# Performance work log

Hardware: AMD Instinct MI355X
Metric: run time of the kernel (lower is better)

## Reference

```python
import jax, jax.numpy as jnp
import numpy as np

B, T, L, D, H = 8, 4, 512, 512, 8
HD = D // H
THR = 1.0
BETA = 0.5
EPS = 1e-5


def heaviside(x):
    return (x >= 0).astype(x.dtype)


def bn_eval(x, g, b, rm, rv):
    # BatchNorm1d in eval mode applied on the last dim
    return (x - rm) * (g * jax.lax.rsqrt(rv + EPS)) + b


def lif(x_btld):
    # snntorch Leaky(beta=0.5, threshold=1, reset='subtract'), mem init 0, scan over T
    xs = jnp.moveaxis(x_btld, 1, 0)  # (T,B,L,D)

    def step(mem, xt):
        reset = heaviside(mem - THR)          # reset from previous mem (detached in torch)
        mem = BETA * mem + xt - reset * THR
        spk = heaviside(mem - THR)
        return mem, spk

    _, spks = jax.lax.scan(step, jnp.zeros_like(xs[0]), xs)
    return jnp.moveaxis(spks, 0, 1)


def setup_inputs() -> dict:
    key = jax.random.key(0)
    ks = jax.random.split(key, 24)
    s = D ** -0.5
    inp = {
        "x": jax.random.normal(ks[0], (B, T, L, D), jnp.float32),
        "q_w": jax.random.normal(ks[1], (D, D), jnp.float32) * s,
        "q_g": jax.random.normal(ks[2], (D,), jnp.float32),
        "q_b": jax.random.normal(ks[3], (D,), jnp.float32),
        "q_rm": jax.random.normal(ks[4], (D,), jnp.float32),
        "q_rv": jax.random.uniform(ks[5], (D,), jnp.float32),
        "k_w": jax.random.normal(ks[6], (D, D), jnp.float32) * s,
        "k_g": jax.random.normal(ks[7], (D,), jnp.float32),
        "k_b": jax.random.normal(ks[8], (D,), jnp.float32),
        "k_rm": jax.random.normal(ks[9], (D,), jnp.float32),
        "k_rv": jax.random.uniform(ks[10], (D,), jnp.float32),
        "v_w": jax.random.normal(ks[11], (D, D), jnp.float32) * s,
        "v_g": jax.random.normal(ks[12], (D,), jnp.float32),
        "v_b": jax.random.normal(ks[13], (D,), jnp.float32),
        "v_rm": jax.random.normal(ks[14], (D,), jnp.float32),
        "v_rv": jax.random.uniform(ks[15], (D,), jnp.float32),
        "o_w": jax.random.normal(ks[16], (D, D), jnp.float32) * s,
        "o_bias": jax.random.normal(ks[17], (D,), jnp.float32),
        "o_g": jax.random.normal(ks[18], (D,), jnp.float32),
        "o_b": jax.random.normal(ks[19], (D,), jnp.float32),
        "o_rm": jax.random.normal(ks[20], (D,), jnp.float32),
        "o_rv": jax.random.uniform(ks[21], (D,), jnp.float32),
    }
    return inp


def reference(x, q_w, q_g, q_b, q_rm, q_rv, k_w, k_g, k_b, k_rm, k_rv,
              v_w, v_g, v_b, v_rm, v_rv, o_w, o_bias, o_g, o_b, o_rm, o_rv):
    scale = HD ** -0.5
    # Q path: linear -> BN -> LIF (binary {0,1})
    q = bn_eval(jnp.einsum('btld,ed->btle', x, q_w), q_g, q_b, q_rm, q_rv)
    q = lif(q)
    # K path: linear -> BN -> ReLU (continuous)
    k = jax.nn.relu(bn_eval(jnp.einsum('btld,ed->btle', x, k_w), k_g, k_b, k_rm, k_rv))
    # V path: linear -> BN -> ternary {-1,0,+1}
    v = bn_eval(jnp.einsum('btld,ed->btle', x, v_w), v_g, v_b, v_rm, v_rv)
    v = heaviside(v - THR) - heaviside(-v - THR)
    # split heads: (B,T,H,L,hd)
    sh = lambda a: a.reshape(B, T, L, H, HD).transpose(0, 1, 3, 2, 4)
    q, k, v = sh(q), sh(k), sh(v)
    attn = jnp.einsum('bthld,bthmd->bthlm', q, k) * scale
    out = jnp.einsum('bthlm,bthmd->bthld', attn, v)
    out = out.transpose(0, 1, 3, 2, 4).reshape(B, T, L, D)
    out = jnp.einsum('btld,ed->btle', out, o_w) + o_bias
    out = bn_eval(out, o_g, o_b, o_rm, o_rv)
    return lif(out)
```

## Files before the change

kernel.cpp:

```cpp
#include <hip/hip_runtime.h>
#include <math.h>
#include <stdint.h>

#define Bb 8
#define Tt 4
#define Ll 512
#define Dd 512
#define Hh 8
#define HDd 64
#define Mm (Bb*Tt*Ll)

typedef _Float16 f16;
typedef _Float16 f16x8 __attribute__((ext_vector_type(8)));
typedef float f32x4 __attribute__((ext_vector_type(4)));

#define LO_SCALE 2048.0f
#define LO_INV   4.8828125e-4f

__device__ __forceinline__ void gload16(const void* g, void* l) {
  __builtin_amdgcn_global_load_lds(
      (const __attribute__((address_space(1))) unsigned int*)(uintptr_t)g,
      (__attribute__((address_space(3))) unsigned int*)(uintptr_t)l,
      16, 0, 0);
}

struct SplitArgs {
  const float* src[5];
  f16* hi[5];
  f16* lo[5];
};

__global__ void split_k(SplitArgs s) {
  int i = blockIdx.x * 256 + threadIdx.x;
  int seg, base;
  if (i < 1048576) { seg = 0; base = i; }
  else { int r = i - 1048576; seg = 1 + (r >> 15); base = r & 32767; }
  const float* sp = s.src[seg] + (size_t)base * 8;
  float4 v0 = *(const float4*)sp;
  float4 v1 = *(const float4*)(sp + 4);
  float a[8] = {v0.x, v0.y, v0.z, v0.w, v1.x, v1.y, v1.z, v1.w};
  f16x8 hv, lv;
  #pragma unroll
  for (int e = 0; e < 8; ++e) {
    f16 hh = (f16)a[e];
    hv[e] = hh;
    lv[e] = (f16)((a[e] - (float)hh) * LO_SCALE);
  }
  *(f16x8*)(s.hi[seg] + (size_t)base * 8) = hv;
  *(f16x8*)(s.lo[seg] + (size_t)base * 8) = lv;
}

struct GArgs {
  const f16 *Ah, *Al;
  const f16 *Wh0, *Wl0, *Wh1, *Wl1, *Wh2, *Wl2;
  const float *g0,*b0,*rm0,*rv0;
  const float *g1,*b1,*rm1,*rv1;
  const float *g2,*b2,*rm2,*rv2;
  const float* bias;
  float *o0, *o1, *o2;
};

template<int MODE>
__global__ __launch_bounds__(256, 2)
void gemm_f16(GArgs ar) {
  __shared__ __align__(16) f16 Ah_s[4096];
  __shared__ __align__(16) f16 Al_s[4096];
  __shared__ __align__(16) f16 Bh_s[4096];
  __shared__ __align__(16) f16 Bl_s[4096];

  const int tid = threadIdx.x;
  const int lane = tid & 63, wid = tid >> 6;
  const int bx = blockIdx.x, by = blockIdx.y;
  const int seg = (MODE == 0) ? (bx >> 2) : 0;
  const int lc0 = (MODE == 0) ? ((bx & 3) << 7) : (bx << 7);
  const int m0 = by << 7;

  const f16* Wh = (seg == 0 ? ar.Wh0 : (seg == 1 ? ar.Wh1 : ar.Wh2));
  const f16* Wl = (seg == 0 ? ar.Wl0 : (seg == 1 ? ar.Wl1 : ar.Wl2));
  const float* gp  = (seg == 0 ? ar.g0  : (seg == 1 ? ar.g1  : ar.g2));
  const float* bp  = (seg == 0 ? ar.b0  : (seg == 1 ? ar.b1  : ar.b2));
  const float* rmp = (seg == 0 ? ar.rm0 : (seg == 1 ? ar.rm1 : ar.rm2));
  const float* rvp = (seg == 0 ? ar.rv0 : (seg == 1 ? ar.rv1 : ar.rv2));
  float* outp = (seg == 0 ? ar.o0 : (seg == 1 ? ar.o1 : ar.o2));

  const int srow = lane >> 2, skc = lane & 3;
  const int fr = lane & 15, kg = lane >> 4;
  const int wmr = wid >> 1, wnc = wid & 1;

  f32x4 acc_h[4][4], acc_l[4][4];
  #pragma unroll
  for (int i = 0; i < 4; ++i)
    #pragma unroll
    for (int j = 0; j < 4; ++j) {
      acc_h[i][j] = (f32x4)0.0f;
      acc_l[i][j] = (f32x4)0.0f;
    }

  for (int k0 = 0; k0 < Dd; k0 += 32) {
    __syncthreads();
    #pragma unroll
    for (int i = 0; i < 2; ++i) {
      const int r = i * 64 + wid * 16 + srow;
      const size_t goA = (size_t)(m0 + r) * Dd + k0 + skc * 8;
      const size_t goB = (size_t)(lc0 + r) * Dd + k0 + skc * 8;
      const int lbase = i * 2048 + wid * 512;
      gload16(ar.Ah + goA, Ah_s + lbase);
      gload16(ar.Al + goA, Al_s + lbase);
      gload16(Wh + goB, Bh_s + lbase);
      gload16(Wl + goB, Bl_s + lbase);
    }
    __syncthreads();

    f16x8 a_h[4], a_l[4], b_h[4], b_l[4];
    #pragma unroll
    for (int i = 0; i < 4; ++i) {
      const int ra = (wmr * 64 + i * 16 + fr) * 32 + kg * 8;
      a_h[i] = *(const f16x8*)&Ah_s[ra];
      a_l[i] = *(const f16x8*)&Al_s[ra];
      const int rb = (wnc * 64 + i * 16 + fr) * 32 + kg * 8;
      b_h[i] = *(const f16x8*)&Bh_s[rb];
      b_l[i] = *(const f16x8*)&Bl_s[rb];
    }
    #pragma unroll
    for (int i = 0; i < 4; ++i)
      #pragma unroll
      for (int j = 0; j < 4; ++j) {
        acc_h[i][j] = __builtin_amdgcn_mfma_f32_16x16x32_f16(a_h[i], b_h[j], acc_h[i][j], 0, 0, 0);
        acc_l[i][j] = __builtin_amdgcn_mfma_f32_16x16x32_f16(a_h[i], b_l[j], acc_l[i][j], 0, 0, 0);
        acc_l[i][j] = __builtin_amdgcn_mfma_f32_16x16x32_f16(a_l[i], b_h[j], acc_l[i][j], 0, 0, 0);
      }
  }

  float scl[4], shc[4];
  #pragma unroll
  for (int j = 0; j < 4; ++j) {
    const int c = lc0 + wnc * 64 + j * 16 + fr;
    double S = (double)gp[c] / sqrt((double)rvp[c] + 1e-5);
    double Sh = (double)bp[c] - (double)rmp[c] * S;
    if (MODE == 1) Sh += (double)ar.bias[c] * S;
    scl[j] = (float)S; shc[j] = (float)Sh;
  }

  #pragma unroll
  for (int i = 0; i < 4; ++i)
    #pragma unroll
    for (int r = 0; r < 4; ++r) {
      const int row = m0 + wmr * 64 + i * 16 + kg * 4 + r;
      #pragma unroll
      for (int j = 0; j < 4; ++j) {
        const int col = lc0 + wnc * 64 + j * 16 + fr;
        float val = acc_h[i][j][r] + acc_l[i][j][r] * LO_INV;
        float y = val * scl[j] + shc[j];
        if (MODE == 0) {
          if (seg == 1) y = fmaxf(y, 0.f);
          else if (seg == 2) y = (y >= 1.f ? 1.f : 0.f) - (-y >= 1.f ? 1.f : 0.f);
        }
        outp[(size_t)row * Dd + col] = y;
      }
    }
}

__global__ void lif_k(float* __restrict__ buf) {
  const int N4 = Bb * Ll * Dd / 4;
  int i = blockIdx.x * blockDim.x + threadIdx.x;
  if (i >= N4) return;
  const int PB = Ll * Dd / 4;
  int b = i >> 16;
  int r = i & 65535;
  float4* p0 = (float4*)buf + (size_t)b * Tt * PB + r;
  float m0 = 0.f, m1 = 0.f, m2 = 0.f, m3 = 0.f;
  #pragma unroll
  for (int t = 0; t < Tt; ++t) {
    float4* p = p0 + (size_t)t * PB;
    float4 xv = *p;
    float4 s;
    { float rst = (m0 >= 1.f) ? 1.f : 0.f; m0 = 0.5f * m0 + xv.x - rst; s.x = (m0 >= 1.f) ? 1.f : 0.f; }
    { float rst = (m1 >= 1.f) ? 1.f : 0.f; m1 = 0.5f * m1 + xv.y - rst; s.y = (m1 >= 1.f) ? 1.f : 0.f; }
    { float rst = (m2 >= 1.f) ? 1.f : 0.f; m2 = 0.5f * m2 + xv.z - rst; s.z = (m2 >= 1.f) ? 1.f : 0.f; }
    { float rst = (m3 >= 1.f) ? 1.f : 0.f; m3 = 0.5f * m3 + xv.w - rst; s.w = (m3 >= 1.f) ? 1.f : 0.f; }
    *p = s;
  }
}

__global__ __launch_bounds__(256)
void attn_g(const float* __restrict__ ks, const float* __restrict__ vs,
            float* __restrict__ pG) {
  const int bt = blockIdx.x, h = blockIdx.y, c = blockIdx.z;
  const float* kp = ks + (size_t)bt * Ll * Dd + h * HDd;
  const float* vp = vs + (size_t)bt * Ll * Dd + h * HDd;

  __shared__ float KS[64][68];
  __shared__ float VS[64][68];
  const int tid = threadIdx.x;
  const int te = tid & 15, td = tid >> 4;

  float gacc[4][4];
  #pragma unroll
  for (int i = 0; i < 4; ++i)
    #pragma unroll
    for (int j = 0; j < 4; ++j) gacc[i][j] = 0.f;

  for (int mt = 0; mt < 2; ++mt) {
    const int m0 = c * 128 + mt * 64;
    #pragma unroll
    for (int it = 0; it < 4; ++it) {
      int fidx = it * 256 + tid;
      int row = fidx >> 4, fq = fidx & 15;
      *(float4*)&KS[row][fq << 2] = *(const float4*)(kp + (size_t)(m0 + row) * Dd + (fq << 2));
      *(float4*)&VS[row][fq << 2] = *(const float4*)(vp + (size_t)(m0 + row) * Dd + (fq << 2));
    }
    __syncthreads();
    #pragma unroll 4
    for (int mm = 0; mm < 64; ++mm) {
      float4 k4 = *(const float4*)&KS[mm][te << 2];
      float4 v4 = *(const float4*)&VS[mm][td << 2];
      const float kk[4] = {k4.x, k4.y, k4.z, k4.w};
      const float vv[4] = {v4.x, v4.y, v4.z, v4.w};
      #pragma unroll
      for (int i = 0; i < 4; ++i)
        #pragma unroll
        for (int j = 0; j < 4; ++j)
          gacc[i][j] = fmaf(kk[i], vv[j], gacc[i][j]);
    }
    __syncthreads();
  }
  float* out = pG + (((size_t)(bt * 8 + h) * 4 + c) << 12);
  #pragma unroll
  for (int i = 0; i < 4; ++i)
    *(float4*)&out[((te << 2) + i) * 64 + (td << 2)] =
        make_float4(gacc[i][0] * 0.125f, gacc[i][1] * 0.125f,
                    gacc[i][2] * 0.125f, gacc[i][3] * 0.125f);
}

__global__ __launch_bounds__(256)
void attn_o(const float* __restrict__ qs, const float* __restrict__ pG,
            f16* __restrict__ ahi, f16* __restrict__ alo) {
  const int bt = blockIdx.x, h = blockIdx.y, lc = blockIdx.z;
  __shared__ float G[64][68];
  __shared__ float QS[64][68];
  const int tid = threadIdx.x;

  const float* pg = pG + (((size_t)(bt * 8 + h) * 4) << 12);
  #pragma unroll
  for (int rep = 0; rep < 4; ++rep) {
    int t4 = rep * 256 + tid;
    int e = t4 >> 4, dq = t4 & 15;
    int off = e * 64 + (dq << 2);
    float4 s0 = *(const float4*)(pg + off);
    float4 s1 = *(const float4*)(pg + 4096 + off);
    float4 s2 = *(const float4*)(pg + 8192 + off);
    float4 s3 = *(const float4*)(pg + 12288 + off);
    *(float4*)&G[e][dq << 2] = make_float4(s0.x + s1.x + s2.x + s3.x,
                                           s0.y + s1.y + s2.y + s3.y,
                                           s0.z + s1.z + s2.z + s3.z,
                                           s0.w + s1.w + s2.w + s3.w);
  }
  __syncthreads();

  const float* qp = qs + (size_t)bt * Ll * Dd + h * HDd;
  const int lr = tid >> 2, dg = tid & 3;

  for (int l0 = 0; l0 < 128; l0 += 64) {
    #pragma unroll
    for (int it = 0; it < 4; ++it) {
      int fidx = it * 256 + tid;
      int row = fidx >> 4, fq = fidx & 15;
      *(float4*)&QS[row][fq << 2] =
          *(const float4*)(qp + (size_t)(lc * 128 + l0 + row) * Dd + (fq << 2));
    }
    __syncthreads();
    float oacc[16];
    #pragma unroll
    for (int j = 0; j < 16; ++j) oacc[j] = 0.f;
    for (int ee = 0; ee < 64; ++ee) {
      float qv = QS[lr][ee];
      #pragma unroll
      for (int jq = 0; jq < 4; ++jq) {
        float4 g4 = *(const float4*)&G[ee][(dg << 4) + (jq << 2)];
        oacc[jq * 4 + 0] = fmaf(qv, g4.x, oacc[jq * 4 + 0]);
        oacc[jq * 4 + 1] = fmaf(qv, g4.y, oacc[jq * 4 + 1]);
        oacc[jq * 4 + 2] = fmaf(qv, g4.z, oacc[jq * 4 + 2]);
        oacc[jq * 4 + 3] = fmaf(qv, g4.w, oacc[jq * 4 + 3]);
      }
    }
    f16x8 h0, l0v, h1, l1v;
    #pragma unroll
    for (int t = 0; t < 8; ++t) {
      float v = oacc[t];
      f16 hh = (f16)v;
      h0[t] = hh; l0v[t] = (f16)((v - (float)hh) * LO_SCALE);
      float v2 = oacc[8 + t];
      f16 hh2 = (f16)v2;
      h1[t] = hh2; l1v[t] = (f16)((v2 - (float)hh2) * LO_SCALE);
    }
    size_t ob = ((size_t)bt * Ll + lc * 128 + l0 + lr) * Dd + h * HDd + (dg << 4);
    *(f16x8*)(ahi + ob) = h0;
    *(f16x8*)(ahi + ob + 8) = h1;
    *(f16x8*)(alo + ob) = l0v;
    *(f16x8*)(alo + ob + 8) = l1v;
    __syncthreads();
  }
}

extern "C" void kernel_launch(void* const* d_in, const int* in_sizes, int n_in,
                              void* d_out, int out_size, void* d_ws, size_t ws_size,
                              hipStream_t stream) {
  const float* x    = (const float*)d_in[0];
  const float* q_w  = (const float*)d_in[1];
  const float* q_g  = (const float*)d_in[2];
  const float* q_b  = (const float*)d_in[3];
  const float* q_rm = (const float*)d_in[4];
  const float* q_rv = (const float*)d_in[5];
  const float* k_w  = (const float*)d_in[6];
  const float* k_g  = (const float*)d_in[7];
  const float* k_b  = (const float*)d_in[8];
  const float* k_rm = (const float*)d_in[9];
  const float* k_rv = (const float*)d_in[10];
  const float* v_w  = (const float*)d_in[11];
  const float* v_g  = (const float*)d_in[12];
  const float* v_b  = (const float*)d_in[13];
  const float* v_rm = (const float*)d_in[14];
  const float* v_rv = (const float*)d_in[15];
  const float* o_w  = (const float*)d_in[16];
  const float* o_bias = (const float*)d_in[17];
  const float* o_g  = (const float*)d_in[18];
  const float* o_b  = (const float*)d_in[19];
  const float* o_rm = (const float*)d_in[20];
  const float* o_rv = (const float*)d_in[21];

  float* ws = (float*)d_ws;
  const size_t NBUF = (size_t)Mm * Dd;
  float* q_lin = ws;
  float* kbuf  = ws + NBUF;
  float* vbuf  = ws + 2 * NBUF;
  float* reg3  = ws + 3 * NBUF;
  f16* xhi = (f16*)reg3;
  f16* xlo = xhi + NBUF;
  float* pG = reg3;
  f16* wsp = (f16*)(ws + 4 * NBUF);
  f16* qwh = wsp;            f16* qwl = wsp + 262144;
  f16* kwh = wsp + 2*262144; f16* kwl = wsp + 3*262144;
  f16* vwh = wsp + 4*262144; f16* vwl = wsp + 5*262144;
  f16* owh = wsp + 6*262144; f16* owl = wsp + 7*262144;
  f16* ahi = (f16*)kbuf;
  f16* alo = ahi + NBUF;
  float* obuf = (float*)d_out;

  SplitArgs sa;
  sa.src[0] = x;   sa.hi[0] = xhi; sa.lo[0] = xlo;
  sa.src[1] = q_w; sa.hi[1] = qwh; sa.lo[1] = qwl;
  sa.src[2] = k_w; sa.hi[2] = kwh; sa.lo[2] = kwl;
  sa.src[3] = v_w; sa.hi[3] = vwh; sa.lo[3] = vwl;
  sa.src[4] = o_w; sa.hi[4] = owh; sa.lo[4] = owl;
  split_k<<<4608, 256, 0, stream>>>(sa);

  GArgs a1;
  a1.Ah = xhi; a1.Al = xlo;
  a1.Wh0 = qwh; a1.Wl0 = qwl; a1.Wh1 = kwh; a1.Wl1 = kwl; a1.Wh2 = vwh; a1.Wl2 = vwl;
  a1.g0 = q_g; a1.b0 = q_b; a1.rm0 = q_rm; a1.rv0 = q_rv;
  a1.g1 = k_g; a1.b1 = k_b; a1.rm1 = k_rm; a1.rv1 = k_rv;
  a1.g2 = v_g; a1.b2 = v_b; a1.rm2 = v_rm; a1.rv2 = v_rv;
  a1.bias = nullptr;
  a1.o0 = q_lin; a1.o1 = kbuf; a1.o2 = vbuf;
  gemm_f16<0><<<dim3(12, 128), 256, 0, stream>>>(a1);

  lif_k<<<2048, 256, 0, stream>>>(q_lin);

  attn_g<<<dim3(32, 8, 4), 256, 0, stream>>>(kbuf, vbuf, pG);
  attn_o<<<dim3(32, 8, 4), 256, 0, stream>>>(q_lin, pG, ahi, alo);

  GArgs a2;
  a2.Ah = ahi; a2.Al = alo;
  a2.Wh0 = owh; a2.Wl0 = owl; a2.Wh1 = owh; a2.Wl1 = owl; a2.Wh2 = owh; a2.Wl2 = owl;
  a2.g0 = o_g; a2.b0 = o_b; a2.rm0 = o_rm; a2.rv0 = o_rv;
  a2.g1 = o_g; a2.b1 = o_b; a2.rm1 = o_rm; a2.rv1 = o_rv;
  a2.g2 = o_g; a2.b2 = o_b; a2.rm2 = o_rm; a2.rv2 = o_rv;
  a2.bias = o_bias;
  a2.o0 = obuf; a2.o1 = obuf; a2.o2 = obuf;
  gemm_f16<1><<<dim3(4, 128), 256, 0, stream>>>(a2);

  lif_k<<<2048, 256, 0, stream>>>(obuf);
}
```

Before: 313.0 us.

## Fuse LIF scan into GEMM epilogues and store binary spikes as fp16

Each GEMM block's M tile is remapped so it covers all 4 timesteps of 32 L-rows for one batch. The LIF recurrence can then run in the epilogue through a shared-memory transpose, and the two standalone lif_k passes are removed. Q spikes and ternary V are stored as fp16 instead of fp32, which cuts write and read traffic for the attention kernels. This costs extra shared memory, added barriers and an LDS transpose in the epilogue, and A-row loads are no longer contiguous 128-row blocks.

```diff
diff --git a/kernel.cpp b/kernel.cpp
--- a/kernel.cpp
+++ b/kernel.cpp
@@ -12,6 +12,7 @@
 
 typedef _Float16 f16;
 typedef _Float16 f16x8 __attribute__((ext_vector_type(8)));
+typedef _Float16 f16x4 __attribute__((ext_vector_type(4)));
 typedef float f32x4 __attribute__((ext_vector_type(4)));
 
 #define LO_SCALE 2048.0f
@@ -57,23 +58,30 @@
   const float *g1,*b1,*rm1,*rv1;
   const float *g2,*b2,*rm2,*rv2;
   const float* bias;
-  float *o0, *o1, *o2;
+  f16*   oq;
+  float* ok;
+  f16*   ov;
+  float* oo;
 };
+
+#define SMEM_BYTES 34048
 
 template<int MODE>
 __global__ __launch_bounds__(256, 2)
 void gemm_f16(GArgs ar) {
-  __shared__ __align__(16) f16 Ah_s[4096];
-  __shared__ __align__(16) f16 Al_s[4096];
-  __shared__ __align__(16) f16 Bh_s[4096];
-  __shared__ __align__(16) f16 Bl_s[4096];
+  extern __shared__ __align__(16) char smem[];
+  f16* Ah_s = (f16*)smem;
+  f16* Al_s = (f16*)(smem + 8192);
+  f16* Bh_s = (f16*)(smem + 16384);
+  f16* Bl_s = (f16*)(smem + 24576);
+  float (*TS)[133] = (float(*)[133])smem;
 
   const int tid = threadIdx.x;
   const int lane = tid & 63, wid = tid >> 6;
   const int bx = blockIdx.x, by = blockIdx.y;
   const int seg = (MODE == 0) ? (bx >> 2) : 0;
   const int lc0 = (MODE == 0) ? ((bx & 3) << 7) : (bx << 7);
-  const int m0 = by << 7;
+  const int b = by >> 4, lc32 = by & 15;
 
   const f16* Wh = (seg == 0 ? ar.Wh0 : (seg == 1 ? ar.Wh1 : ar.Wh2));
   const f16* Wl = (seg == 0 ? ar.Wl0 : (seg == 1 ? ar.Wl1 : ar.Wl2));
@@ -81,7 +89,6 @@
   const float* bp  = (seg == 0 ? ar.b0  : (seg == 1 ? ar.b1  : ar.b2));
   const float* rmp = (seg == 0 ? ar.rm0 : (seg == 1 ? ar.rm1 : ar.rm2));
   const float* rvp = (seg == 0 ? ar.rv0 : (seg == 1 ? ar.rv1 : ar.rv2));
-  float* outp = (seg == 0 ? ar.o0 : (seg == 1 ? ar.o1 : ar.o2));
 
   const int srow = lane >> 2, skc = lane & 3;
   const int fr = lane & 15, kg = lane >> 4;
@@ -101,7 +108,8 @@
     #pragma unroll
     for (int i = 0; i < 2; ++i) {
       const int r = i * 64 + wid * 16 + srow;
-      const size_t goA = (size_t)(m0 + r) * Dd + k0 + skc * 8;
+      const int grow = (((b << 2) + (r >> 5)) << 9) + (lc32 << 5) + (r & 31);
+      const size_t goA = (size_t)grow * Dd + k0 + skc * 8;
       const size_t goB = (size_t)(lc0 + r) * Dd + k0 + skc * 8;
       const int lbase = i * 2048 + wid * 512;
       gload16(ar.Ah + goA, Ah_s + lbase);
@@ -141,53 +149,82 @@
     scl[j] = (float)S; shc[j] = (float)Sh;
   }
 
-  #pragma unroll
-  for (int i = 0; i < 4; ++i)
-    #pragma unroll
-    for (int r = 0; r < 4; ++r) {
-      const int row = m0 + wmr * 64 + i * 16 + kg * 4 + r;
-      #pragma unroll
-      for (int j = 0; j < 4; ++j) {
-        const int col = lc0 + wnc * 64 + j * 16 + fr;
-        float val = acc_h[i][j][r] + acc_l[i][j][r] * LO_INV;
-        float y = val * scl[j] + shc[j];
+  if (MODE == 0 && seg != 0) {
+    #pragma unroll
+    for (int i = 0; i < 4; ++i)
+      #pragma unroll
+      for (int r = 0; r < 4; ++r) {
+        const int tr = wmr * 64 + i * 16 + (kg << 2) + r;
+        const int grow = (((b << 2) + (tr >> 5)) << 9) + (lc32 << 5) + (tr & 31);
+        #pragma unroll
+        for (int j = 0; j < 4; ++j) {
+          const int col = lc0 + wnc * 64 + j * 16 + fr;
+          float val = acc_h[i][j][r] + acc_l[i][j][r] * LO_INV;
+          float y = val * scl[j] + shc[j];
+          if (seg == 1) ar.ok[(size_t)grow * Dd + col] = fmaxf(y, 0.f);
+          else ar.ov[(size_t)grow * Dd + col] =
+                   (f16)((y >= 1.f ? 1.f : 0.f) - (-y >= 1.f ? 1.f : 0.f));
+        }
+      }
+    return;
+  }
+
+  __syncthreads();
+  #pragma unroll
+  for (int half = 0; half < 2; ++half) {
+    if (wnc == half) {
+      #pragma unroll
+      for (int i = 0; i < 4; ++i)
+        #pragma unroll
+        for (int j = 0; j < 4; ++j) {
+          float4 yv;
+          float* yp = &yv.x;
+          #pragma unroll
+          for (int r = 0; r < 4; ++r) {
+            float val = acc_h[i][j][r] + acc_l[i][j][r] * LO_INV;
+            yp[r] = val * scl[j] + shc[j];
+          }
+          *(float4*)&TS[j * 16 + fr][wmr * 64 + i * 16 + (kg << 2)] = yv;
+        }
+    }
+    __syncthreads();
+    const int cc4 = (tid & 15) << 2;
+    #pragma unroll
+    for (int rr = 0; rr < 2; ++rr) {
+      const int rl = (tid >> 4) + (rr << 4);
+      float mm[4] = {0.f, 0.f, 0.f, 0.f};
+      #pragma unroll
+      for (int t = 0; t < 4; ++t) {
+        const int trow = t * 32 + rl;
+        float sp[4];
+        #pragma unroll
+        for (int c = 0; c < 4; ++c) {
+          float y = TS[cc4 + c][trow];
+          float rst = (mm[c] >= 1.f) ? 1.f : 0.f;
+          mm[c] = 0.5f * mm[c] + y - rst;
+          sp[c] = (mm[c] >= 1.f) ? 1.f : 0.f;
+        }
+        const size_t go = ((size_t)((((b << 2) + t) << 9) + (lc32 << 5) + rl)) * Dd
+                          + lc0 + (half << 6) + cc4;
         if (MODE == 0) {
-          if (seg == 1) y = fmaxf(y, 0.f);
-          else if (seg == 2) y = (y >= 1.f ? 1.f : 0.f) - (-y >= 1.f ? 1.f : 0.f);
+          f16x4 s4;
+          s4[0] = (f16)sp[0]; s4[1] = (f16)sp[1]; s4[2] = (f16)sp[2]; s4[3] = (f16)sp[3];
+          *(f16x4*)(ar.oq + go) = s4;
+        } else {
+          *(float4*)(ar.oo + go) = make_float4(sp[0], sp[1], sp[2], sp[3]);
         }
-        outp[(size_t)row * Dd + col] = y;
       }
     }
-}
-
-__global__ void lif_k(float* __restrict__ buf) {
-  const int N4 = Bb * Ll * Dd / 4;
-  int i = blockIdx.x * blockDim.x + threadIdx.x;
-  if (i >= N4) return;
-  const int PB = Ll * Dd / 4;
-  int b = i >> 16;
-  int r = i & 65535;
-  float4* p0 = (float4*)buf + (size_t)b * Tt * PB + r;
-  float m0 = 0.f, m1 = 0.f, m2 = 0.f, m3 = 0.f;
-  #pragma unroll
-  for (int t = 0; t < Tt; ++t) {
-    float4* p = p0 + (size_t)t * PB;
-    float4 xv = *p;
-    float4 s;
-    { float rst = (m0 >= 1.f) ? 1.f : 0.f; m0 = 0.5f * m0 + xv.x - rst; s.x = (m0 >= 1.f) ? 1.f : 0.f; }
-    { float rst = (m1 >= 1.f) ? 1.f : 0.f; m1 = 0.5f * m1 + xv.y - rst; s.y = (m1 >= 1.f) ? 1.f : 0.f; }
-    { float rst = (m2 >= 1.f) ? 1.f : 0.f; m2 = 0.5f * m2 + xv.z - rst; s.z = (m2 >= 1.f) ? 1.f : 0.f; }
-    { float rst = (m3 >= 1.f) ? 1.f : 0.f; m3 = 0.5f * m3 + xv.w - rst; s.w = (m3 >= 1.f) ? 1.f : 0.f; }
-    *p = s;
+    __syncthreads();
   }
 }
 
 __global__ __launch_bounds__(256)
-void attn_g(const float* __restrict__ ks, const float* __restrict__ vs,
+void attn_g(const float* __restrict__ ks, const f16* __restrict__ vs,
             float* __restrict__ pG) {
   const int bt = blockIdx.x, h = blockIdx.y, c = blockIdx.z;
   const float* kp = ks + (size_t)bt * Ll * Dd + h * HDd;
-  const float* vp = vs + (size_t)bt * Ll * Dd + h * HDd;
+  const f16* vp = vs + (size_t)bt * Ll * Dd + h * HDd;
 
   __shared__ float KS[64][68];
   __shared__ float VS[64][68];
@@ -207,7 +244,14 @@
       int fidx = it * 256 + tid;
       int row = fidx >> 4, fq = fidx & 15;
       *(float4*)&KS[row][fq << 2] = *(const float4*)(kp + (size_t)(m0 + row) * Dd + (fq << 2));
-      *(float4*)&VS[row][fq << 2] = *(const float4*)(vp + (size_t)(m0 + row) * Dd + (fq << 2));
+    }
+    #pragma unroll
+    for (int it = 0; it < 2; ++it) {
+      int fidx = it * 256 + tid;
+      int row = fidx >> 3, c8 = fidx & 7;
+      f16x8 hv = *(const f16x8*)(vp + (size_t)(m0 + row) * Dd + (c8 << 3));
+      *(float4*)&VS[row][c8 << 3] = make_float4(hv[0], hv[1], hv[2], hv[3]);
+      *(float4*)&VS[row][(c8 << 3) + 4] = make_float4(hv[4], hv[5], hv[6], hv[7]);
     }
     __syncthreads();
     #pragma unroll 4
@@ -233,7 +277,7 @@
 }
 
 __global__ __launch_bounds__(256)
-void attn_o(const float* __restrict__ qs, const float* __restrict__ pG,
+void attn_o(const f16* __restrict__ qs, const float* __restrict__ pG,
             f16* __restrict__ ahi, f16* __restrict__ alo) {
   const int bt = blockIdx.x, h = blockIdx.y, lc = blockIdx.z;
   __shared__ float G[64][68];
@@ -257,16 +301,17 @@
   }
   __syncthreads();
 
-  const float* qp = qs + (size_t)bt * Ll * Dd + h * HDd;
+  const f16* qp = qs + (size_t)bt * Ll * Dd + h * HDd;
   const int lr = tid >> 2, dg = tid & 3;
 
   for (int l0 = 0; l0 < 128; l0 += 64) {
     #pragma unroll
-    for (int it = 0; it < 4; ++it) {
+    for (int it = 0; it < 2; ++it) {
       int fidx = it * 256 + tid;
-      int row = fidx >> 4, fq = fidx & 15;
-      *(float4*)&QS[row][fq << 2] =
-          *(const float4*)(qp + (size_t)(lc * 128 + l0 + row) * Dd + (fq << 2));
+      int row = fidx >> 3, c8 = fidx & 7;
+      f16x8 hv = *(const f16x8*)(qp + (size_t)(lc * 128 + l0 + row) * Dd + (c8 << 3));
+      *(float4*)&QS[row][c8 << 3] = make_float4(hv[0], hv[1], hv[2], hv[3]);
+      *(float4*)&QS[row][(c8 << 3) + 4] = make_float4(hv[4], hv[5], hv[6], hv[7]);
     }
     __syncthreads();
     float oacc[16];
@@ -328,23 +373,21 @@
   const float* o_rm = (const float*)d_in[20];
   const float* o_rv = (const float*)d_in[21];
 
-  float* ws = (float*)d_ws;
-  const size_t NBUF = (size_t)Mm * Dd;
-  float* q_lin = ws;
-  float* kbuf  = ws + NBUF;
-  float* vbuf  = ws + 2 * NBUF;
-  float* reg3  = ws + 3 * NBUF;
-  f16* xhi = (f16*)reg3;
-  f16* xlo = xhi + NBUF;
-  float* pG = reg3;
-  f16* wsp = (f16*)(ws + 4 * NBUF);
+  char* wsb = (char*)d_ws;
+  const size_t R16 = 16777216;
+  f16*   xhi  = (f16*)wsb;
+  f16*   xlo  = (f16*)(wsb + R16);
+  f16*   qspk = (f16*)(wsb + 2 * R16);
+  float* kbuf = (float*)(wsb + 3 * R16);
+  f16*   vbuf = (f16*)(wsb + 5 * R16);
+  float* pG   = (float*)(wsb + 6 * R16);
+  f16*   wsp  = (f16*)(wsb + 7 * R16);
   f16* qwh = wsp;            f16* qwl = wsp + 262144;
   f16* kwh = wsp + 2*262144; f16* kwl = wsp + 3*262144;
   f16* vwh = wsp + 4*262144; f16* vwl = wsp + 5*262144;
   f16* owh = wsp + 6*262144; f16* owl = wsp + 7*262144;
-  f16* ahi = (f16*)kbuf;
-  f16* alo = ahi + NBUF;
-  float* obuf = (float*)d_out;
+  f16* ahi = xhi;
+  f16* alo = xlo;
 
   SplitArgs sa;
   sa.src[0] = x;   sa.hi[0] = xhi; sa.lo[0] = xlo;
@@ -361,13 +404,11 @@
   a1.g1 = k_g; a1.b1 = k_b; a1.rm1 = k_rm; a1.rv1 = k_rv;
   a1.g2 = v_g; a1.b2 = v_b; a1.rm2 = v_rm; a1.rv2 = v_rv;
   a1.bias = nullptr;
-  a1.o0 = q_lin; a1.o1 = kbuf; a1.o2 = vbuf;
-  gemm_f16<0><<<dim3(12, 128), 256, 0, stream>>>(a1);
-
-  lif_k<<<2048, 256, 0, stream>>>(q_lin);
+  a1.oq = qspk; a1.ok = kbuf; a1.ov = vbuf; a1.oo = nullptr;
+  gemm_f16<0><<<dim3(12, 128), 256, SMEM_BYTES, stream>>>(a1);
 
   attn_g<<<dim3(32, 8, 4), 256, 0, stream>>>(kbuf, vbuf, pG);
-  attn_o<<<dim3(32, 8, 4), 256, 0, stream>>>(q_lin, pG, ahi, alo);
+  attn_o<<<dim3(32, 8, 4), 256, 0, stream>>>(qspk, pG, ahi, alo);
 
   GArgs a2;
   a2.Ah = ahi; a2.Al = alo;
@@ -376,8 +417,6 @@
   a2.g1 = o_g; a2.b1 = o_b; a2.rm1 = o_rm; a2.rv1 = o_rv;
   a2.g2 = o_g; a2.b2 = o_b; a2.rm2 = o_rm; a2.rv2 = o_rv;
   a2.bias = o_bias;
-  a2.o0 = obuf; a2.o1 = obuf; a2.o2 = obuf;
-  gemm_f16<1><<<dim3(4, 128), 256, 0, stream>>>(a2);
-
-  lif_k<<<2048, 256, 0, stream>>>(obuf);
-}
+  a2.oq = nullptr; a2.ok = nullptr; a2.ov = nullptr; a2.oo = (float*)d_out;
+  gemm_f16<1><<<dim3(4, 128), 256, SMEM_BYTES, stream>>>(a2);
+}
```

Result: faster. 302.6 us (-3.3%).
